# Kernel optimization log

Hardware: AMD Instinct MI355X
Metric: run time of the kernel (lower is better)

The kernel has to match this reference:

```python
import jax, jax.numpy as jnp
import numpy as np

N = 100000
E = 3200000
G = 256


def _glorot(key, shape):
    lim = float(np.sqrt(6.0 / (shape[0] + shape[1])))
    return jax.random.uniform(key, shape, jnp.float32, -lim, lim)


def setup_inputs() -> dict:
    key = jax.random.key(0)
    ks = jax.random.split(key, 16)
    x = jax.random.normal(ks[0], (N, 128), jnp.float32)
    edge_index = jax.random.randint(ks[1], (2, E), 0, N, jnp.int64)
    batch = jnp.sort(jax.random.randint(ks[2], (N,), 0, G, jnp.int64))
    inp = {
        'x': x, 'edge_index': edge_index, 'batch': batch,
        'enc_w1': _glorot(ks[3], (128, 128)), 'enc_b1': jnp.zeros((128,), jnp.float32),
        'enc_w2': _glorot(ks[4], (128, 64)),  'enc_b2': jnp.zeros((64,), jnp.float32),
        'w1': _glorot(ks[5], (64, 64)), 'b1': jnp.zeros((64,), jnp.float32),
        'w2': _glorot(ks[6], (64, 64)), 'b2': jnp.zeros((64,), jnp.float32),
        'w3': _glorot(ks[7], (64, 64)), 'b3': jnp.zeros((64,), jnp.float32),
        'sg_w': _glorot(ks[8], (64, 64)), 'sg_b': jnp.zeros((64,), jnp.float32),
        'fc1_w': _glorot(ks[9], (64, 32)), 'fc1_b': jnp.zeros((32,), jnp.float32),
        'fc2_w': _glorot(ks[10], (32, 16)), 'fc2_b': jnp.zeros((16,), jnp.float32),
        'cpd_w': _glorot(ks[11], (16, 1)), 'cpd_b': jnp.zeros((1,), jnp.float32),
        'comb_w': _glorot(ks[12], (16, 1)), 'comb_b': jnp.zeros((1,), jnp.float32),
    }
    return inp


def _gcn_edges(edge_index, n):
    # add self loops, compute symmetric normalization deg^-1/2 * deg^-1/2
    loop = jnp.arange(n, dtype=edge_index.dtype)
    src = jnp.concatenate([edge_index[0], loop])
    dst = jnp.concatenate([edge_index[1], loop])
    deg = jax.ops.segment_sum(jnp.ones_like(dst, dtype=jnp.float32), dst, num_segments=n)
    dinv = jnp.where(deg > 0, jax.lax.rsqrt(deg), 0.0)
    norm = dinv[src] * dinv[dst]  # [E+N]
    return src, dst, norm


def _propagate(h, src, dst, norm, n):
    # gather -> scale -> scatter-add (normalized neighbor aggregation)
    return jax.ops.segment_sum(h[src] * norm[:, None], dst, num_segments=n)


def _gcn_conv(h, w, b, src, dst, norm, n):
    return _propagate(h @ w, src, dst, norm, n) + b


def reference(x, edge_index, batch, enc_w1, enc_b1, enc_w2, enc_b2,
              w1, b1, w2, b2, w3, b3, sg_w, sg_b,
              fc1_w, fc1_b, fc2_w, fc2_b, cpd_w, cpd_b, comb_w, comb_b):
    n = x.shape[0]
    src, dst, norm = _gcn_edges(edge_index, n)
    # encoder
    z = jax.nn.relu(_gcn_conv(x, enc_w1, enc_b1, src, dst, norm, n))
    z = _gcn_conv(z, enc_w2, enc_b2, src, dst, norm, n)
    z = jax.nn.relu(_gcn_conv(z, w1, b1, src, dst, norm, n))
    z = jax.nn.relu(_gcn_conv(z, w2, b2, src, dst, norm, n))
    z = jax.nn.relu(_gcn_conv(z, w3, b3, src, dst, norm, n))
    for _ in range(4):
        z = _propagate(z, src, dst, norm, n)
    z = z @ sg_w + sg_b
    # global max pool over graphs
    z = jax.ops.segment_max(z, batch, num_segments=G)  # [G, 64]
    z = jax.nn.relu(z @ fc1_w + fc1_b)
    z = jax.nn.relu(z @ fc2_w + fc2_b)
    cpd_pred = z @ cpd_w + cpd_b
    comb_logits = z @ comb_w + comb_b
    return (cpd_pred, comb_logits)
```

## Files before the change

### kernel.cpp

```cpp
#include <hip/hip_runtime.h>
#include <hip/hip_fp16.h>
#include <cfloat>
#include <type_traits>

#define DEV __device__ __forceinline__

DEV unsigned enc_ord(float f) {
    unsigned u = __float_as_uint(f);
    return (u & 0x80000000u) ? ~u : (u | 0x80000000u);
}

__global__ __launch_bounds__(256) void k_bcount(const int* __restrict__ dst, int* __restrict__ bcnt, int E) {
    __shared__ int hist[256];
    int tid = threadIdx.x;
    hist[tid] = 0;
    __syncthreads();
    int base = blockIdx.x * 4096;
#pragma unroll
    for (int j = 0; j < 16; ++j) {
        int e = base + j * 256 + tid;
        if (e < E) atomicAdd(&hist[dst[e] >> 9], 1);
    }
    __syncthreads();
    if (hist[tid]) atomicAdd(&bcnt[tid], hist[tid]);
}

__global__ __launch_bounds__(256) void k_bscan(const int* __restrict__ bcnt, int* __restrict__ bbase,
                                               int* __restrict__ bcur, int* __restrict__ rowptr,
                                               int nb, int n, int E) {
    __shared__ int sh[256];
    int tid = threadIdx.x;
    int v = (tid < nb) ? bcnt[tid] : 0;
    sh[tid] = v; __syncthreads();
    for (int off = 1; off < 256; off <<= 1) {
        int x = (tid >= off) ? sh[tid - off] : 0; __syncthreads();
        sh[tid] += x; __syncthreads();
    }
    int excl = sh[tid] - v;
    if (tid < nb) { bbase[tid] = excl; bcur[tid] = excl; }
    if (tid == 0) { bbase[nb] = E; rowptr[n] = E; }
}

__global__ __launch_bounds__(256) void k_bscatter(const int* __restrict__ ei, int* __restrict__ bcur,
                                                  int2* __restrict__ pairs, int E) {
    __shared__ int hist[256];
    __shared__ int gbase[256];
    int tid = threadIdx.x;
    hist[tid] = 0;
    __syncthreads();
    int base = blockIdx.x * 4096;
    int d[16], li[16];
#pragma unroll
    for (int j = 0; j < 16; ++j) {
        int e = base + j * 256 + tid;
        if (e < E) {
            d[j] = ei[E + e];
            li[j] = atomicAdd(&hist[d[j] >> 9], 1);
        }
    }
    __syncthreads();
    if (hist[tid]) gbase[tid] = atomicAdd(&bcur[tid], hist[tid]);
    __syncthreads();
#pragma unroll
    for (int j = 0; j < 16; ++j) {
        int e = base + j * 256 + tid;
        if (e < E) {
            int b = d[j] >> 9;
            pairs[gbase[b] + li[j]] = make_int2(ei[e], d[j]);
        }
    }
}

__global__ __launch_bounds__(512) void k_bfill(const int2* __restrict__ pairs, const int* __restrict__ bbase,
                                               int* __restrict__ rowptr, float* __restrict__ dinv,
                                               int* __restrict__ colA, int n) {
    __shared__ int sdeg[512];
    __shared__ int scur[512];
    int tid = threadIdx.x;
    int b = blockIdx.x;
    int bb = bbase[b], be = bbase[b + 1];
    int nodeBase = b << 9;
    sdeg[tid] = 0;
    __syncthreads();
    for (int e = bb + tid; e < be; e += 512) {
        int2 pr = pairs[e];
        atomicAdd(&sdeg[pr.y & 511], 1);
    }
    __syncthreads();
    int v = sdeg[tid];
    __syncthreads();
    sdeg[tid] = v; __syncthreads();
    for (int off = 1; off < 512; off <<= 1) {
        int x = (tid >= off) ? sdeg[tid - off] : 0; __syncthreads();
        sdeg[tid] += x; __syncthreads();
    }
    int excl = sdeg[tid] - v;
    scur[tid] = excl;
    int node = nodeBase + tid;
    if (node < n) {
        rowptr[node] = bb + excl;
        dinv[node] = rsqrtf((float)v + 1.0f);
    }
    __syncthreads();
    for (int e = bb + tid; e < be; e += 512) {
        int2 pr = pairs[e];
        int p = atomicAdd(&scur[pr.y & 511], 1);
        colA[bb + p] = pr.x;
    }
}

template <int K, int COUT, bool SCALE, bool BIAS, typename TIN, typename TOUT>
__global__ __launch_bounds__(256) void k_mm(const TIN* __restrict__ in, const float* __restrict__ W,
                                            const float* __restrict__ bias, const float* __restrict__ dinv,
                                            TOUT* __restrict__ out, int n, int ldw, int ldo, int colOff) {
    constexpr int CG = COUT / 4;
    constexpr int SLOTS = 256 / CG;
    constexpr int TR = (K == 128) ? 32 : 64;
    constexpr int RPT = TR / SLOTS;
    constexpr int KP = K + 1;
    __shared__ __align__(16) float sW[K * COUT];
    __shared__ float sH[TR * KP];
    const int tid = threadIdx.x;
    const int rowBase = blockIdx.x * TR;

    constexpr int W4 = COUT / 4;
    for (int idx = tid; idx < K * W4; idx += 256) {
        int k = idx / W4, c4 = idx - k * W4;
        ((float4*)sW)[idx] = *(const float4*)(W + (size_t)k * ldw + colOff + c4 * 4);
    }
    if constexpr (std::is_same<TIN, float>::value) {
        const float4* inp4 = (const float4*)(in + (size_t)rowBase * K);
        for (int idx = tid; idx < TR * K / 4; idx += 256) {
            int elem = idx * 4;
            int r = elem / K, k = elem - r * K;
            float4 h = (rowBase + r < n) ? inp4[idx] : make_float4(0.f, 0.f, 0.f, 0.f);
            float* dd = &sH[r * KP + k];
            dd[0] = h.x; dd[1] = h.y; dd[2] = h.z; dd[3] = h.w;
        }
    } else {
        const uint4* inp8 = (const uint4*)(in + (size_t)rowBase * K);
        for (int idx = tid; idx < TR * K / 8; idx += 256) {
            int elem = idx * 8;
            int r = elem / K, k = elem - r * K;
            uint4 h = make_uint4(0u, 0u, 0u, 0u);
            if (rowBase + r < n) h = inp8[idx];
            const __half2* hh = (const __half2*)&h;
            float* dd = &sH[r * KP + k];
#pragma unroll
            for (int q = 0; q < 4; ++q) {
                float2 f = __half22float2(hh[q]);
                dd[2 * q] = f.x; dd[2 * q + 1] = f.y;
            }
        }
    }
    __syncthreads();

    const int cg = tid % CG;
    const int slot = tid / CG;
    float4 acc[RPT];
#pragma unroll
    for (int j = 0; j < RPT; ++j) acc[j] = make_float4(0.f, 0.f, 0.f, 0.f);
#pragma unroll 4
    for (int k = 0; k < K; ++k) {
        float4 w = *(const float4*)&sW[k * COUT + cg * 4];
#pragma unroll
        for (int j = 0; j < RPT; ++j) {
            float h = sH[(slot + j * SLOTS) * KP + k];
            acc[j].x += h * w.x; acc[j].y += h * w.y; acc[j].z += h * w.z; acc[j].w += h * w.w;
        }
    }
#pragma unroll
    for (int j = 0; j < RPT; ++j) {
        int r = rowBase + slot + j * SLOTS;
        if (r < n) {
            float4 o = acc[j];
            if (SCALE) { float di = dinv[r]; o.x *= di; o.y *= di; o.z *= di; o.w *= di; }
            if (BIAS) {
                float4 b = *(const float4*)(bias + colOff + cg * 4);
                o.x += b.x; o.y += b.y; o.z += b.z; o.w += b.w;
            }
            if constexpr (std::is_same<TOUT, float>::value) {
                *(float4*)(out + (size_t)r * ldo + colOff + cg * 4) = o;
            } else {
                __half2 p0 = __floats2half2_rn(o.x, o.y);
                __half2 p1 = __floats2half2_rn(o.z, o.w);
                uint2 st;
                st.x = *(unsigned*)&p0; st.y = *(unsigned*)&p1;
                *(uint2*)(out + (size_t)r * ldo + colOff + cg * 4) = st;
            }
        }
    }
}

template <int WIDTH, int MODE>
__global__ __launch_bounds__(256) void k_agg(const __half* __restrict__ g, const int* __restrict__ rowptr,
                                             const int* __restrict__ col, const float* __restrict__ dinv,
                                             const float* __restrict__ bias, __half* __restrict__ out, int n) {
    constexpr int LPR = WIDTH / 8;
    constexpr int RPW = 64 / LPR;
    int gw = (blockIdx.x * 256 + threadIdx.x) >> 6;
    int lane = threadIdx.x & 63;
    int seg = lane / LPR;
    int sl = lane % LPR;
    int row = gw * RPW + seg;
    if (row >= n) return;
    const uint4* g4 = (const uint4*)g + sl;
    float acc[8];
    {
        uint4 s = g4[(size_t)row * LPR];
        const __half2* h = (const __half2*)&s;
#pragma unroll
        for (int q = 0; q < 4; ++q) {
            float2 f = __half22float2(h[q]);
            acc[2 * q] = f.x; acc[2 * q + 1] = f.y;
        }
    }
    int e0 = rowptr[row], e1 = rowptr[row + 1];
    if (e0 < e1) {
        const int e1m1 = e1 - 1;
        int c[8];
#pragma unroll
        for (int j = 0; j < 8; ++j) c[j] = col[min(e0 + j, e1m1)];
        for (int eb = e0; eb < e1; eb += 8) {
            uint4 v[8];
#pragma unroll
            for (int j = 0; j < 8; ++j) v[j] = g4[(size_t)c[j] * LPR];
            int cn[8];
#pragma unroll
            for (int j = 0; j < 8; ++j) cn[j] = col[min(eb + 8 + j, e1m1)];
            int rem = e1 - eb;
#pragma unroll
            for (int j = 0; j < 8; ++j) {
                float m = (j < rem) ? 1.f : 0.f;
                const __half2* h = (const __half2*)&v[j];
#pragma unroll
                for (int q = 0; q < 4; ++q) {
                    float2 f = __half22float2(h[q]);
                    acc[2 * q]     = fmaf(m, f.x, acc[2 * q]);
                    acc[2 * q + 1] = fmaf(m, f.y, acc[2 * q + 1]);
                }
            }
#pragma unroll
            for (int j = 0; j < 8; ++j) c[j] = cn[j];
        }
    }
    float di = dinv[row];
    float r8[8];
    if (MODE == 0 || MODE == 1 || MODE == 2) {
        float4 b0 = *(const float4*)(bias + sl * 8);
        float4 b1 = *(const float4*)(bias + sl * 8 + 4);
        float bb[8] = {b0.x, b0.y, b0.z, b0.w, b1.x, b1.y, b1.z, b1.w};
#pragma unroll
        for (int t = 0; t < 8; ++t) {
            float s = di * acc[t] + bb[t];
            if (MODE == 0) r8[t] = fmaxf(s, 0.f);
            else if (MODE == 1) r8[t] = s;
            else r8[t] = di * fmaxf(s, 0.f);
        }
    } else if (MODE == 3) {
        float d2 = di * di;
#pragma unroll
        for (int t = 0; t < 8; ++t) r8[t] = acc[t] * d2;
    } else {
#pragma unroll
        for (int t = 0; t < 8; ++t) r8[t] = acc[t] * di;
    }
    uint4 o;
    __half2* oh = (__half2*)&o;
#pragma unroll
    for (int q = 0; q < 4; ++q) oh[q] = __floats2half2_rn(r8[2 * q], r8[2 * q + 1]);
    *((uint4*)out + (size_t)row * LPR + sl) = o;
}

__global__ __launch_bounds__(64) void k_pool(const float* __restrict__ z, const int* __restrict__ batch,
                                             unsigned* __restrict__ pooled, int n) {
    constexpr int ROWS = 128;
    int lane = threadIdx.x;
    int r0 = blockIdx.x * ROWS;
    if (r0 >= n) return;
    int r1 = min(r0 + ROWS, n);
    int cur = batch[r0];
    float m = -FLT_MAX;
    for (int r = r0; r < r1; ++r) {
        int b = batch[r];
        float v = z[(size_t)r * 64 + lane];
        if (b != cur) {
            atomicMax(&pooled[cur * 64 + lane], enc_ord(m));
            cur = b; m = v;
        } else {
            m = fmaxf(m, v);
        }
    }
    atomicMax(&pooled[cur * 64 + lane], enc_ord(m));
}

__global__ __launch_bounds__(256) void k_mlp(const unsigned* __restrict__ pooled,
                                             const float* __restrict__ fc1w, const float* __restrict__ fc1b,
                                             const float* __restrict__ fc2w, const float* __restrict__ fc2b,
                                             const float* __restrict__ cpdw, const float* __restrict__ cpdb,
                                             const float* __restrict__ combw, const float* __restrict__ combb,
                                             float* __restrict__ out, int G) {
    __shared__ float s1[64 * 32], s2[32 * 16], sb1[32], sb2[16], scw[16], sow[16], shead[2];
    int tid = threadIdx.x;
    for (int i = tid; i < 2048; i += 256) s1[i] = fc1w[i];
    for (int i = tid; i < 512; i += 256) s2[i] = fc2w[i];
    if (tid < 32) sb1[tid] = fc1b[tid];
    if (tid < 16) { sb2[tid] = fc2b[tid]; scw[tid] = cpdw[tid]; sow[tid] = combw[tid]; }
    if (tid == 0) { shead[0] = cpdb[0]; shead[1] = combb[0]; }
    __syncthreads();
    if (tid < G) {
        float h0[64];
#pragma unroll
        for (int k = 0; k < 64; ++k) {
            unsigned u = pooled[tid * 64 + k];
            unsigned b = (u & 0x80000000u) ? (u & 0x7fffffffu) : ~u;
            h0[k] = __uint_as_float(b);
        }
        float h1[32];
#pragma unroll
        for (int j = 0; j < 32; ++j) {
            float a = sb1[j];
#pragma unroll
            for (int k = 0; k < 64; ++k) a += h0[k] * s1[k * 32 + j];
            h1[j] = fmaxf(a, 0.f);
        }
        float h2[16];
#pragma unroll
        for (int j = 0; j < 16; ++j) {
            float a = sb2[j];
#pragma unroll
            for (int k = 0; k < 32; ++k) a += h1[k] * s2[k * 16 + j];
            h2[j] = fmaxf(a, 0.f);
        }
        float c1 = shead[0], c2 = shead[1];
#pragma unroll
        for (int k = 0; k < 16; ++k) { c1 += h2[k] * scw[k]; c2 += h2[k] * sow[k]; }
        out[tid] = c1;
        out[G + tid] = c2;
    }
}

extern "C" void kernel_launch(void* const* d_in, const int* in_sizes, int n_in,
                              void* d_out, int out_size, void* d_ws, size_t ws_size,
                              hipStream_t stream) {
    const float* x      = (const float*)d_in[0];
    const int*   ei     = (const int*)d_in[1];
    const int*   batch  = (const int*)d_in[2];
    const float* enc_w1 = (const float*)d_in[3];
    const float* enc_b1 = (const float*)d_in[4];
    const float* enc_w2 = (const float*)d_in[5];
    const float* enc_b2 = (const float*)d_in[6];
    const float* w1 = (const float*)d_in[7];   const float* b1 = (const float*)d_in[8];
    const float* w2 = (const float*)d_in[9];   const float* b2 = (const float*)d_in[10];
    const float* w3 = (const float*)d_in[11];  const float* b3 = (const float*)d_in[12];
    const float* sgw = (const float*)d_in[13]; const float* sgb = (const float*)d_in[14];
    const float* fc1w = (const float*)d_in[15]; const float* fc1b = (const float*)d_in[16];
    const float* fc2w = (const float*)d_in[17]; const float* fc2b = (const float*)d_in[18];
    const float* cpdw = (const float*)d_in[19]; const float* cpdb = (const float*)d_in[20];
    const float* combw = (const float*)d_in[21]; const float* combb = (const float*)d_in[22];

    const int n = in_sizes[0] / 128;
    const int E = in_sizes[1] / 2;
    const int G = out_size / 2;
    const int nb = (n + 511) >> 9;
    float* outp = (float*)d_out;

    char* p = (char*)d_ws;
    auto alloc = [&](size_t bytes) -> char* {
        char* r = p;
        p += (bytes + 255) & ~(size_t)255;
        return r;
    };
    int* rowptr      = (int*)alloc((size_t)(n + 1) * 4);
    float* dinv      = (float*)alloc((size_t)n * 4);
    int* bcnt        = (int*)alloc(256 * 4);
    int* bbase       = (int*)alloc(257 * 4);
    int* bcur        = (int*)alloc(256 * 4);
    int* colA        = (int*)alloc((size_t)E * 4);
    unsigned* pooled = (unsigned*)alloc((size_t)G * 64 * 4);
    __half* A        = (__half*)alloc((size_t)n * 128 * 4);
    __half* B        = (__half*)alloc((size_t)n * 128 * 2);
    float* Cf        = (float*)alloc((size_t)n * 64 * 4);
    int2* pairs      = (int2*)A;

    hipMemsetAsync(bcnt, 0, 256 * 4, stream);
    hipMemsetAsync(pooled, 0, (size_t)G * 64 * 4, stream);

    const int gE = (E + 4095) / 4096;
    k_bcount<<<gE, 256, 0, stream>>>(ei + E, bcnt, E);
    k_bscan<<<1, 256, 0, stream>>>(bcnt, bbase, bcur, rowptr, nb, n, E);
    k_bscatter<<<gE, 256, 0, stream>>>(ei, bcur, pairs, E);
    k_bfill<<<nb, 512, 0, stream>>>(pairs, bbase, rowptr, dinv, colA, n);

    const int gm128 = (n + 31) / 32;
    const int gm64  = (n + 63) / 64;
    const int ga64  = (n + 31) / 32;
    const int ga128 = (n + 15) / 16;

    k_mm<128, 64, true, false, float, __half><<<gm128, 256, 0, stream>>>(x, enc_w1, nullptr, dinv, A, n, 128, 128, 0);
    k_mm<128, 64, true, false, float, __half><<<gm128, 256, 0, stream>>>(x, enc_w1, nullptr, dinv, A, n, 128, 128, 64);
    k_agg<128, 0><<<ga128, 256, 0, stream>>>(A, rowptr, colA, dinv, enc_b1, B, n);
    k_mm<128, 64, true, false, __half, __half><<<gm128, 256, 0, stream>>>(B, enc_w2, nullptr, dinv, A, n, 64, 64, 0);
    k_agg<64, 1><<<ga64, 256, 0, stream>>>(A, rowptr, colA, dinv, enc_b2, B, n);
    k_mm<64, 64, true, false, __half, __half><<<gm64, 256, 0, stream>>>(B, w1, nullptr, dinv, A, n, 64, 64, 0);
    k_agg<64, 0><<<ga64, 256, 0, stream>>>(A, rowptr, colA, dinv, b1, B, n);
    k_mm<64, 64, true, false, __half, __half><<<gm64, 256, 0, stream>>>(B, w2, nullptr, dinv, A, n, 64, 64, 0);
    k_agg<64, 0><<<ga64, 256, 0, stream>>>(A, rowptr, colA, dinv, b2, B, n);
    k_mm<64, 64, true, false, __half, __half><<<gm64, 256, 0, stream>>>(B, w3, nullptr, dinv, A, n, 64, 64, 0);
    k_agg<64, 2><<<ga64, 256, 0, stream>>>(A, rowptr, colA, dinv, b3, B, n);
    k_agg<64, 3><<<ga64, 256, 0, stream>>>(B, rowptr, colA, dinv, b3, A, n);
    k_agg<64, 3><<<ga64, 256, 0, stream>>>(A, rowptr, colA, dinv, b3, B, n);
    k_agg<64, 3><<<ga64, 256, 0, stream>>>(B, rowptr, colA, dinv, b3, A, n);
    k_agg<64, 4><<<ga64, 256, 0, stream>>>(A, rowptr, colA, dinv, b3, B, n);
    k_mm<64, 64, false, true, __half, float><<<gm64, 256, 0, stream>>>(B, sgw, sgb, dinv, Cf, n, 64, 64, 0);
    k_pool<<<(n + 127) / 128, 64, 0, stream>>>(Cf, batch, pooled, n);
    k_mlp<<<1, 256, 0, stream>>>(pooled, fc1w, fc1b, fc2w, fc2b, cpdw, cpdb, combw, combb, outp, G);
}
```

Baseline: 1.008 ms.

## Partition CSR edges by source-node range and aggregate in cache-local phases

```diff
diff --git a/kernel.cpp b/kernel.cpp
--- a/kernel.cpp
+++ b/kernel.cpp
@@ -9,6 +9,7 @@
     unsigned u = __float_as_uint(f);
     return (u & 0x80000000u) ? ~u : (u | 0x80000000u);
 }
+
 
 __global__ __launch_bounds__(256) void k_bcount(const int* __restrict__ dst, int* __restrict__ bcnt, int E) {
     __shared__ int hist[256];
@@ -73,39 +74,46 @@
 
 __global__ __launch_bounds__(512) void k_bfill(const int2* __restrict__ pairs, const int* __restrict__ bbase,
                                                int* __restrict__ rowptr, float* __restrict__ dinv,
-                                               int* __restrict__ colA, int n) {
-    __shared__ int sdeg[512];
-    __shared__ int scur[512];
+                                               int* __restrict__ colA, int* __restrict__ pp, int n) {
+    __shared__ int sdeg2[512 * 8];
+    __shared__ int scur2[512 * 8];
+    __shared__ int ssum[512];
     int tid = threadIdx.x;
     int b = blockIdx.x;
     int bb = bbase[b], be = bbase[b + 1];
     int nodeBase = b << 9;
-    sdeg[tid] = 0;
+    for (int i = tid; i < 4096; i += 512) sdeg2[i] = 0;
     __syncthreads();
     for (int e = bb + tid; e < be; e += 512) {
         int2 pr = pairs[e];
-        atomicAdd(&sdeg[pr.y & 511], 1);
-    }
-    __syncthreads();
-    int v = sdeg[tid];
-    __syncthreads();
-    sdeg[tid] = v; __syncthreads();
+        atomicAdd(&sdeg2[(pr.y & 511) * 8 + (pr.x >> 14)], 1);
+    }
+    __syncthreads();
+    int vals[8], ex[8];
+    int tsum = 0;
+#pragma unroll
+    for (int q = 0; q < 8; ++q) { vals[q] = sdeg2[tid * 8 + q]; ex[q] = tsum; tsum += vals[q]; }
+    ssum[tid] = tsum; __syncthreads();
     for (int off = 1; off < 512; off <<= 1) {
-        int x = (tid >= off) ? sdeg[tid - off] : 0; __syncthreads();
-        sdeg[tid] += x; __syncthreads();
-    }
-    int excl = sdeg[tid] - v;
-    scur[tid] = excl;
+        int x = (tid >= off) ? ssum[tid - off] : 0; __syncthreads();
+        ssum[tid] += x; __syncthreads();
+    }
+    int excl = ssum[tid] - tsum;
+#pragma unroll
+    for (int q = 0; q < 8; ++q) scur2[tid * 8 + q] = excl + ex[q];
     int node = nodeBase + tid;
     if (node < n) {
         rowptr[node] = bb + excl;
-        dinv[node] = rsqrtf((float)v + 1.0f);
+        dinv[node] = rsqrtf((float)tsum + 1.0f);
+#pragma unroll
+        for (int q = 0; q < 8; ++q) pp[(size_t)node * 8 + q] = bb + excl + ex[q];
     }
     __syncthreads();
     for (int e = bb + tid; e < be; e += 512) {
         int2 pr = pairs[e];
-        int p = atomicAdd(&scur[pr.y & 511], 1);
-        colA[bb + p] = pr.x;
+        int idx = (pr.y & 511) * 8 + (pr.x >> 14);
+        int p2 = atomicAdd(&scur2[idx], 1);
+        colA[bb + p2] = pr.x;
     }
 }
 
@@ -192,12 +200,12 @@
     }
 }
 
-template <int WIDTH, int MODE>
-__global__ __launch_bounds__(256) void k_agg(const __half* __restrict__ g, const int* __restrict__ rowptr,
-                                             const int* __restrict__ col, const float* __restrict__ dinv,
-                                             const float* __restrict__ bias, __half* __restrict__ out, int n) {
-    constexpr int LPR = WIDTH / 8;
-    constexpr int RPW = 64 / LPR;
+template <int MODE>
+__global__ __launch_bounds__(256) void k_agg128(const __half* __restrict__ g, const int* __restrict__ rowptr,
+                                                const int* __restrict__ col, const float* __restrict__ dinv,
+                                                const float* __restrict__ bias, __half* __restrict__ out, int n) {
+    constexpr int LPR = 16;
+    constexpr int RPW = 4;
     int gw = (blockIdx.x * 256 + threadIdx.x) >> 6;
     int lane = threadIdx.x & 63;
     int seg = lane / LPR;
@@ -224,20 +232,21 @@
         for (int eb = e0; eb < e1; eb += 8) {
             uint4 v[8];
 #pragma unroll
-            for (int j = 0; j < 8; ++j) v[j] = g4[(size_t)c[j] * LPR];
+            for (int j = 0; j < 8; ++j) {
+                v[j] = make_uint4(0u, 0u, 0u, 0u);
+                if (eb + j < e1) v[j] = g4[(size_t)c[j] * LPR];
+            }
             int cn[8];
 #pragma unroll
             for (int j = 0; j < 8; ++j) cn[j] = col[min(eb + 8 + j, e1m1)];
-            int rem = e1 - eb;
 #pragma unroll
             for (int j = 0; j < 8; ++j) {
-                float m = (j < rem) ? 1.f : 0.f;
                 const __half2* h = (const __half2*)&v[j];
 #pragma unroll
                 for (int q = 0; q < 4; ++q) {
                     float2 f = __half22float2(h[q]);
-                    acc[2 * q]     = fmaf(m, f.x, acc[2 * q]);
-                    acc[2 * q + 1] = fmaf(m, f.y, acc[2 * q + 1]);
+                    acc[2 * q] += f.x;
+                    acc[2 * q + 1] += f.y;
                 }
             }
 #pragma unroll
@@ -246,30 +255,123 @@
     }
     float di = dinv[row];
     float r8[8];
-    if (MODE == 0 || MODE == 1 || MODE == 2) {
-        float4 b0 = *(const float4*)(bias + sl * 8);
-        float4 b1 = *(const float4*)(bias + sl * 8 + 4);
-        float bb[8] = {b0.x, b0.y, b0.z, b0.w, b1.x, b1.y, b1.z, b1.w};
-#pragma unroll
-        for (int t = 0; t < 8; ++t) {
-            float s = di * acc[t] + bb[t];
-            if (MODE == 0) r8[t] = fmaxf(s, 0.f);
-            else if (MODE == 1) r8[t] = s;
-            else r8[t] = di * fmaxf(s, 0.f);
-        }
-    } else if (MODE == 3) {
-        float d2 = di * di;
-#pragma unroll
-        for (int t = 0; t < 8; ++t) r8[t] = acc[t] * d2;
-    } else {
-#pragma unroll
-        for (int t = 0; t < 8; ++t) r8[t] = acc[t] * di;
+    float4 b0 = *(const float4*)(bias + sl * 8);
+    float4 b1 = *(const float4*)(bias + sl * 8 + 4);
+    float bb[8] = {b0.x, b0.y, b0.z, b0.w, b1.x, b1.y, b1.z, b1.w};
+#pragma unroll
+    for (int t = 0; t < 8; ++t) {
+        float s = di * acc[t] + bb[t];
+        r8[t] = (MODE == 0) ? fmaxf(s, 0.f) : s;
     }
     uint4 o;
     __half2* oh = (__half2*)&o;
 #pragma unroll
     for (int q = 0; q < 4; ++q) oh[q] = __floats2half2_rn(r8[2 * q], r8[2 * q + 1]);
     *((uint4*)out + (size_t)row * LPR + sl) = o;
+}
+
+template <int MODE>
+__global__ __launch_bounds__(256) void k_aggp(const __half* __restrict__ g, const int* __restrict__ pp,
+                                              const int* __restrict__ col, const float* __restrict__ dinv,
+                                              const float* __restrict__ bias, __half* __restrict__ out,
+                                              int n, int nPhases) {
+    constexpr int RPB = 224;
+    __shared__ float sacc[RPB * 64];
+    const int tid = threadIdx.x;
+    const int r0 = blockIdx.x * RPB;
+    for (int i = tid; i < RPB * 16; i += 256) {
+        int rr = i >> 4, u = i & 15;
+        int row = r0 + rr;
+        float v0 = 0.f, v1 = 0.f, v2 = 0.f, v3 = 0.f;
+        if (row < n) {
+            uint2 h = *((const uint2*)(g + (size_t)row * 64) + u);
+            __half2 a = *(__half2*)&h.x;
+            __half2 b = *(__half2*)&h.y;
+            float2 fa = __half22float2(a), fb = __half22float2(b);
+            v0 = fa.x; v1 = fa.y; v2 = fb.x; v3 = fb.y;
+        }
+        float* d = &sacc[rr * 64 + u * 4];
+        d[0] = v0; d[1] = v1; d[2] = v2; d[3] = v3;
+    }
+    __syncthreads();
+    const int segid = tid >> 3;
+    const int sl = tid & 7;
+    const uint4* g4 = (const uint4*)g + sl;
+    for (int p = 0; p < nPhases; ++p) {
+        for (int rr = segid; rr < RPB; rr += 32) {
+            int row = r0 + rr;
+            if (row >= n) break;
+            int e0 = pp[(size_t)row * 8 + p];
+            int e1 = pp[(size_t)row * 8 + p + 1];
+            if (e0 >= e1) continue;
+            const int e1m1 = e1 - 1;
+            float acc[8];
+#pragma unroll
+            for (int t = 0; t < 8; ++t) acc[t] = 0.f;
+            int c[8];
+#pragma unroll
+            for (int j = 0; j < 8; ++j) c[j] = col[min(e0 + j, e1m1)];
+            for (int eb = e0; eb < e1; eb += 8) {
+                uint4 v[8];
+#pragma unroll
+                for (int j = 0; j < 8; ++j) {
+                    v[j] = make_uint4(0u, 0u, 0u, 0u);
+                    if (eb + j < e1) v[j] = g4[(size_t)c[j] * 8];
+                }
+                int cn[8];
+#pragma unroll
+                for (int j = 0; j < 8; ++j) cn[j] = col[min(eb + 8 + j, e1m1)];
+#pragma unroll
+                for (int j = 0; j < 8; ++j) {
+                    const __half2* h = (const __half2*)&v[j];
+#pragma unroll
+                    for (int q = 0; q < 4; ++q) {
+                        float2 f = __half22float2(h[q]);
+                        acc[2 * q] += f.x;
+                        acc[2 * q + 1] += f.y;
+                    }
+                }
+#pragma unroll
+                for (int j = 0; j < 8; ++j) c[j] = cn[j];
+            }
+            float* a = &sacc[rr * 64 + sl * 8];
+#pragma unroll
+            for (int t = 0; t < 8; ++t) a[t] += acc[t];
+        }
+        __syncthreads();
+    }
+    for (int i = tid; i < RPB * 8; i += 256) {
+        int rr = i >> 3, q = i & 7;
+        int row = r0 + rr;
+        if (row >= n) break;
+        float di = dinv[row];
+        const float* a = &sacc[rr * 64 + q * 8];
+        float r8[8];
+        if (MODE <= 2) {
+            float4 b0 = *(const float4*)(bias + q * 8);
+            float4 b1 = *(const float4*)(bias + q * 8 + 4);
+            float bb[8] = {b0.x, b0.y, b0.z, b0.w, b1.x, b1.y, b1.z, b1.w};
+#pragma unroll
+            for (int t = 0; t < 8; ++t) {
+                float s = di * a[t] + bb[t];
+                if (MODE == 0) r8[t] = fmaxf(s, 0.f);
+                else if (MODE == 1) r8[t] = s;
+                else r8[t] = di * fmaxf(s, 0.f);
+            }
+        } else if (MODE == 3) {
+            float d2 = di * di;
+#pragma unroll
+            for (int t = 0; t < 8; ++t) r8[t] = a[t] * d2;
+        } else {
+#pragma unroll
+            for (int t = 0; t < 8; ++t) r8[t] = a[t] * di;
+        }
+        uint4 o;
+        __half2* oh = (__half2*)&o;
+#pragma unroll
+        for (int w = 0; w < 4; ++w) oh[w] = __floats2half2_rn(r8[2 * w], r8[2 * w + 1]);
+        *((uint4*)out + (size_t)row * 8 + q) = o;
+    }
 }
 
 __global__ __launch_bounds__(64) void k_pool(const float* __restrict__ z, const int* __restrict__ batch,
@@ -363,6 +465,7 @@
     const int E = in_sizes[1] / 2;
     const int G = out_size / 2;
     const int nb = (n + 511) >> 9;
+    const int nPhases = ((n - 1) >> 14) + 1;
     float* outp = (float*)d_out;
 
     char* p = (char*)d_ws;
@@ -377,6 +480,7 @@
     int* bbase       = (int*)alloc(257 * 4);
     int* bcur        = (int*)alloc(256 * 4);
     int* colA        = (int*)alloc((size_t)E * 4);
+    int* pp          = (int*)alloc((size_t)n * 8 * 4);
     unsigned* pooled = (unsigned*)alloc((size_t)G * 64 * 4);
     __half* A        = (__half*)alloc((size_t)n * 128 * 4);
     __half* B        = (__half*)alloc((size_t)n * 128 * 2);
@@ -390,28 +494,28 @@
     k_bcount<<<gE, 256, 0, stream>>>(ei + E, bcnt, E);
     k_bscan<<<1, 256, 0, stream>>>(bcnt, bbase, bcur, rowptr, nb, n, E);
     k_bscatter<<<gE, 256, 0, stream>>>(ei, bcur, pairs, E);
-    k_bfill<<<nb, 512, 0, stream>>>(pairs, bbase, rowptr, dinv, colA, n);
+    k_bfill<<<nb, 512, 0, stream>>>(pairs, bbase, rowptr, dinv, colA, pp, n);
 
     const int gm128 = (n + 31) / 32;
     const int gm64  = (n + 63) / 64;
-    const int ga64  = (n + 31) / 32;
     const int ga128 = (n + 15) / 16;
+    const int gp    = (n + 223) / 224;
 
     k_mm<128, 64, true, false, float, __half><<<gm128, 256, 0, stream>>>(x, enc_w1, nullptr, dinv, A, n, 128, 128, 0);
     k_mm<128, 64, true, false, float, __half><<<gm128, 256, 0, stream>>>(x, enc_w1, nullptr, dinv, A, n, 128, 128, 64);
-    k_agg<128, 0><<<ga128, 256, 0, stream>>>(A, rowptr, colA, dinv, enc_b1, B, n);
+    k_agg128<0><<<ga128, 256, 0, stream>>>(A, rowptr, colA, dinv, enc_b1, B, n);
     k_mm<128, 64, true, false, __half, __half><<<gm128, 256, 0, stream>>>(B, enc_w2, nullptr, dinv, A, n, 64, 64, 0);
-    k_agg<64, 1><<<ga64, 256, 0, stream>>>(A, rowptr, colA, dinv, enc_b2, B, n);
+    k_aggp<1><<<gp, 256, 0, stream>>>(A, pp, colA, dinv, enc_b2, B, n, nPhases);
     k_mm<64, 64, true, false, __half, __half><<<gm64, 256, 0, stream>>>(B, w1, nullptr, dinv, A, n, 64, 64, 0);
-    k_agg<64, 0><<<ga64, 256, 0, stream>>>(A, rowptr, colA, dinv, b1, B, n);
+    k_aggp<0><<<gp, 256, 0, stream>>>(A, pp, colA, dinv, b1, B, n, nPhases);
     k_mm<64, 64, true, false, __half, __half><<<gm64, 256, 0, stream>>>(B, w2, nullptr, dinv, A, n, 64, 64, 0);
-    k_agg<64, 0><<<ga64, 256, 0, stream>>>(A, rowptr, colA, dinv, b2, B, n);
+    k_aggp<0><<<gp, 256, 0, stream>>>(A, pp, colA, dinv, b2, B, n, nPhases);
     k_mm<64, 64, true, false, __half, __half><<<gm64, 256, 0, stream>>>(B, w3, nullptr, dinv, A, n, 64, 64, 0);
-    k_agg<64, 2><<<ga64, 256, 0, stream>>>(A, rowptr, colA, dinv, b3, B, n);
-    k_agg<64, 3><<<ga64, 256, 0, stream>>>(B, rowptr, colA, dinv, b3, A, n);
-    k_agg<64, 3><<<ga64, 256, 0, stream>>>(A, rowptr, colA, dinv, b3, B, n);
-    k_agg<64, 3><<<ga64, 256, 0, stream>>>(B, rowptr, colA, dinv, b3, A, n);
-    k_agg<64, 4><<<ga64, 256, 0, stream>>>(A, rowptr, colA, dinv, b3, B, n);
+    k_aggp<2><<<gp, 256, 0, stream>>>(A, pp, colA, dinv, b3, B, n, nPhases);
+    k_aggp<3><<<gp, 256, 0, stream>>>(B, pp, colA, dinv, b3, A, n, nPhases);
+    k_aggp<3><<<gp, 256, 0, stream>>>(A, pp, colA, dinv, b3, B, n, nPhases);
+    k_aggp<3><<<gp, 256, 0, stream>>>(B, pp, colA, dinv, b3, A, n, nPhases);
+    k_aggp<4><<<gp, 256, 0, stream>>>(A, pp, colA, dinv, b3, B, n, nPhases);
     k_mm<64, 64, false, true, __half, float><<<gm64, 256, 0, stream>>>(B, sgw, sgb, dinv, Cf, n, 64, 64, 0);
     k_pool<<<(n + 127) / 128, 64, 0, stream>>>(Cf, batch, pooled, n);
     k_mlp<<<1, 256, 0, stream>>>(pooled, fc1w, fc1b, fc2w, fc2b, cpdw, cpdb, combw, combb, outp, G);
```

Result: slower. 1.576 ms (+56.3%).

## Partition CSR edges by source window and process them in phases for gather locality

Applied to the files above, without the earlier changes.

```diff
diff --git a/kernel.cpp b/kernel.cpp
--- a/kernel.cpp
+++ b/kernel.cpp
@@ -10,6 +10,7 @@
     return (u & 0x80000000u) ? ~u : (u | 0x80000000u);
 }
 
+
 __global__ __launch_bounds__(256) void k_bcount(const int* __restrict__ dst, int* __restrict__ bcnt, int E) {
     __shared__ int hist[256];
     int tid = threadIdx.x;
@@ -26,8 +27,7 @@
 }
 
 __global__ __launch_bounds__(256) void k_bscan(const int* __restrict__ bcnt, int* __restrict__ bbase,
-                                               int* __restrict__ bcur, int* __restrict__ rowptr,
-                                               int nb, int n, int E) {
+                                               int* __restrict__ bcur, int nb, int E) {
     __shared__ int sh[256];
     int tid = threadIdx.x;
     int v = (tid < nb) ? bcnt[tid] : 0;
@@ -38,7 +38,7 @@
     }
     int excl = sh[tid] - v;
     if (tid < nb) { bbase[tid] = excl; bcur[tid] = excl; }
-    if (tid == 0) { bbase[nb] = E; rowptr[n] = E; }
+    if (tid == 0) bbase[nb] = E;
 }
 
 __global__ __launch_bounds__(256) void k_bscatter(const int* __restrict__ ei, int* __restrict__ bcur,
@@ -72,40 +72,48 @@
 }
 
 __global__ __launch_bounds__(512) void k_bfill(const int2* __restrict__ pairs, const int* __restrict__ bbase,
-                                               int* __restrict__ rowptr, float* __restrict__ dinv,
-                                               int* __restrict__ colA, int n) {
-    __shared__ int sdeg[512];
-    __shared__ int scur[512];
+                                               float* __restrict__ dinv, int* __restrict__ colA,
+                                               int* __restrict__ pp, int n, int nw) {
+    __shared__ int sdeg2[512 * 16];
+    __shared__ int ssum[512];
     int tid = threadIdx.x;
     int b = blockIdx.x;
     int bb = bbase[b], be = bbase[b + 1];
     int nodeBase = b << 9;
-    sdeg[tid] = 0;
+    for (int i = tid; i < 512 * 16; i += 512) sdeg2[i] = 0;
     __syncthreads();
     for (int e = bb + tid; e < be; e += 512) {
         int2 pr = pairs[e];
-        atomicAdd(&sdeg[pr.y & 511], 1);
-    }
-    __syncthreads();
-    int v = sdeg[tid];
-    __syncthreads();
-    sdeg[tid] = v; __syncthreads();
+        atomicAdd(&sdeg2[(pr.y & 511) * 16 + (pr.x >> 13)], 1);
+    }
+    __syncthreads();
+    int vals[16], ex[16];
+    int tsum = 0;
+#pragma unroll
+    for (int q = 0; q < 16; ++q) {
+        vals[q] = (q < nw) ? sdeg2[tid * 16 + q] : 0;
+        ex[q] = tsum; tsum += vals[q];
+    }
+    ssum[tid] = tsum; __syncthreads();
     for (int off = 1; off < 512; off <<= 1) {
-        int x = (tid >= off) ? sdeg[tid - off] : 0; __syncthreads();
-        sdeg[tid] += x; __syncthreads();
-    }
-    int excl = sdeg[tid] - v;
-    scur[tid] = excl;
+        int x = (tid >= off) ? ssum[tid - off] : 0; __syncthreads();
+        ssum[tid] += x; __syncthreads();
+    }
+    int excl = ssum[tid] - tsum;
+#pragma unroll
+    for (int q = 0; q < 16; ++q) if (q < nw) sdeg2[tid * 16 + q] = excl + ex[q];
     int node = nodeBase + tid;
     if (node < n) {
-        rowptr[node] = bb + excl;
-        dinv[node] = rsqrtf((float)v + 1.0f);
+        dinv[node] = rsqrtf((float)tsum + 1.0f);
+        for (int q = 0; q < nw; ++q) pp[node * 16 + q] = bb + excl + ex[q];
+        pp[node * 16 + nw] = bb + excl + tsum;
     }
     __syncthreads();
     for (int e = bb + tid; e < be; e += 512) {
         int2 pr = pairs[e];
-        int p = atomicAdd(&scur[pr.y & 511], 1);
-        colA[bb + p] = pr.x;
+        int idx = (pr.y & 511) * 16 + (pr.x >> 13);
+        int p2 = atomicAdd(&sdeg2[idx], 1);
+        colA[bb + p2] = pr.x;
     }
 }
 
@@ -193,83 +201,103 @@
 }
 
 template <int WIDTH, int MODE>
-__global__ __launch_bounds__(256) void k_agg(const __half* __restrict__ g, const int* __restrict__ rowptr,
-                                             const int* __restrict__ col, const float* __restrict__ dinv,
-                                             const float* __restrict__ bias, __half* __restrict__ out, int n) {
+__global__ __launch_bounds__(256) void k_aggp(const __half* __restrict__ g, const int* __restrict__ pp,
+                                              const int* __restrict__ col, const float* __restrict__ dinv,
+                                              const float* __restrict__ bias, __half* __restrict__ out,
+                                              int n, int nw) {
     constexpr int LPR = WIDTH / 8;
-    constexpr int RPW = 64 / LPR;
-    int gw = (blockIdx.x * 256 + threadIdx.x) >> 6;
-    int lane = threadIdx.x & 63;
-    int seg = lane / LPR;
-    int sl = lane % LPR;
-    int row = gw * RPW + seg;
-    if (row >= n) return;
+    constexpr int SPW = 64 / LPR;
+    constexpr int RPW = SPW * 4;
+    constexpr int MERGE = (WIDTH == 64) ? 2 : 1;
+    const int tid = threadIdx.x;
+    const int wave = tid >> 6, lane = tid & 63;
+    const int seg = lane / LPR, sl = lane % LPR;
+    const int rowBase = blockIdx.x * (RPW * 4) + wave * RPW + seg * 4;
     const uint4* g4 = (const uint4*)g + sl;
-    float acc[8];
-    {
-        uint4 s = g4[(size_t)row * LPR];
+
+    float acc[4][8];
+#pragma unroll
+    for (int j = 0; j < 4; ++j) {
+        int row = rowBase + j;
+        uint4 s = make_uint4(0u, 0u, 0u, 0u);
+        if (row < n) s = g4[(size_t)row * LPR];
         const __half2* h = (const __half2*)&s;
 #pragma unroll
         for (int q = 0; q < 4; ++q) {
             float2 f = __half22float2(h[q]);
-            acc[2 * q] = f.x; acc[2 * q + 1] = f.y;
-        }
-    }
-    int e0 = rowptr[row], e1 = rowptr[row + 1];
-    if (e0 < e1) {
-        const int e1m1 = e1 - 1;
-        int c[8];
-#pragma unroll
-        for (int j = 0; j < 8; ++j) c[j] = col[min(e0 + j, e1m1)];
-        for (int eb = e0; eb < e1; eb += 8) {
-            uint4 v[8];
-#pragma unroll
-            for (int j = 0; j < 8; ++j) v[j] = g4[(size_t)c[j] * LPR];
-            int cn[8];
-#pragma unroll
-            for (int j = 0; j < 8; ++j) cn[j] = col[min(eb + 8 + j, e1m1)];
-            int rem = e1 - eb;
-#pragma unroll
-            for (int j = 0; j < 8; ++j) {
-                float m = (j < rem) ? 1.f : 0.f;
-                const __half2* h = (const __half2*)&v[j];
-#pragma unroll
-                for (int q = 0; q < 4; ++q) {
-                    float2 f = __half22float2(h[q]);
-                    acc[2 * q]     = fmaf(m, f.x, acc[2 * q]);
-                    acc[2 * q + 1] = fmaf(m, f.y, acc[2 * q + 1]);
+            acc[j][2 * q] = f.x; acc[j][2 * q + 1] = f.y;
+        }
+    }
+
+    const int nPh = (nw + MERGE - 1) / MERGE;
+    for (int p = 0; p < nPh; ++p) {
+        const int lo = p * MERGE;
+        const int hi = min(lo + MERGE, nw);
+#pragma unroll
+        for (int j = 0; j < 4; ++j) {
+            int row = rowBase + j;
+            if (row < n) {
+                int e0 = pp[row * 16 + lo];
+                int e1 = pp[row * 16 + hi];
+                if (e0 < e1) {
+                    const int e1m1 = e1 - 1;
+                    for (int eb = e0; eb < e1; eb += 8) {
+                        int cc[8];
+#pragma unroll
+                        for (int t = 0; t < 8; ++t) cc[t] = col[min(eb + t, e1m1)];
+                        uint4 v[8];
+#pragma unroll
+                        for (int t = 0; t < 8; ++t) {
+                            v[t] = make_uint4(0u, 0u, 0u, 0u);
+                            if (eb + t < e1) v[t] = g4[(size_t)cc[t] * LPR];
+                        }
+#pragma unroll
+                        for (int t = 0; t < 8; ++t) {
+                            const __half2* h = (const __half2*)&v[t];
+#pragma unroll
+                            for (int q = 0; q < 4; ++q) {
+                                float2 f = __half22float2(h[q]);
+                                acc[j][2 * q] += f.x;
+                                acc[j][2 * q + 1] += f.y;
+                            }
+                        }
+                    }
                 }
             }
-#pragma unroll
-            for (int j = 0; j < 8; ++j) c[j] = cn[j];
-        }
-    }
-    float di = dinv[row];
-    float r8[8];
-    if (MODE == 0 || MODE == 1 || MODE == 2) {
-        float4 b0 = *(const float4*)(bias + sl * 8);
-        float4 b1 = *(const float4*)(bias + sl * 8 + 4);
-        float bb[8] = {b0.x, b0.y, b0.z, b0.w, b1.x, b1.y, b1.z, b1.w};
-#pragma unroll
-        for (int t = 0; t < 8; ++t) {
-            float s = di * acc[t] + bb[t];
-            if (MODE == 0) r8[t] = fmaxf(s, 0.f);
-            else if (MODE == 1) r8[t] = s;
-            else r8[t] = di * fmaxf(s, 0.f);
-        }
-    } else if (MODE == 3) {
-        float d2 = di * di;
-#pragma unroll
-        for (int t = 0; t < 8; ++t) r8[t] = acc[t] * d2;
-    } else {
-#pragma unroll
-        for (int t = 0; t < 8; ++t) r8[t] = acc[t] * di;
-    }
-    uint4 o;
-    __half2* oh = (__half2*)&o;
-#pragma unroll
-    for (int q = 0; q < 4; ++q) oh[q] = __floats2half2_rn(r8[2 * q], r8[2 * q + 1]);
-    *((uint4*)out + (size_t)row * LPR + sl) = o;
+        }
+    }
+
+#pragma unroll
+    for (int j = 0; j < 4; ++j) {
+        int row = rowBase + j;
+        if (row >= n) continue;
+        float di = dinv[row];
+        float r8[8];
+        if (MODE <= 2) {
+            float4 b0 = *(const float4*)(bias + sl * 8);
+            float4 b1 = *(const float4*)(bias + sl * 8 + 4);
+            float bb[8] = {b0.x, b0.y, b0.z, b0.w, b1.x, b1.y, b1.z, b1.w};
+#pragma unroll
+            for (int t = 0; t < 8; ++t) {
+                float s = di * acc[j][t] + bb[t];
+                if (MODE == 0) r8[t] = fmaxf(s, 0.f);
+                else if (MODE == 1) r8[t] = s;
+                else r8[t] = di * fmaxf(s, 0.f);
+            }
+        } else if (MODE == 3) {
+            float d2 = di * di;
+#pragma unroll
+            for (int t = 0; t < 8; ++t) r8[t] = acc[j][t] * d2;
+        } else {
+#pragma unroll
+            for (int t = 0; t < 8; ++t) r8[t] = acc[j][t] * di;
+        }
+        uint4 o;
+        __half2* oh = (__half2*)&o;
+#pragma unroll
+        for (int q = 0; q < 4; ++q) oh[q] = __floats2half2_rn(r8[2 * q], r8[2 * q + 1]);
+        *((uint4*)out + (size_t)row * LPR + sl) = o;
+    }
 }
 
 __global__ __launch_bounds__(64) void k_pool(const float* __restrict__ z, const int* __restrict__ batch,
@@ -363,6 +391,7 @@
     const int E = in_sizes[1] / 2;
     const int G = out_size / 2;
     const int nb = (n + 511) >> 9;
+    const int nw = ((n - 1) >> 13) + 1;
     float* outp = (float*)d_out;
 
     char* p = (char*)d_ws;
@@ -371,12 +400,12 @@
         p += (bytes + 255) & ~(size_t)255;
         return r;
     };
-    int* rowptr      = (int*)alloc((size_t)(n + 1) * 4);
     float* dinv      = (float*)alloc((size_t)n * 4);
     int* bcnt        = (int*)alloc(256 * 4);
     int* bbase       = (int*)alloc(257 * 4);
     int* bcur        = (int*)alloc(256 * 4);
     int* colA        = (int*)alloc((size_t)E * 4);
+    int* pp          = (int*)alloc((size_t)n * 16 * 4);
     unsigned* pooled = (unsigned*)alloc((size_t)G * 64 * 4);
     __half* A        = (__half*)alloc((size_t)n * 128 * 4);
     __half* B        = (__half*)alloc((size_t)n * 128 * 2);
@@ -388,30 +417,30 @@
 
     const int gE = (E + 4095) / 4096;
     k_bcount<<<gE, 256, 0, stream>>>(ei + E, bcnt, E);
-    k_bscan<<<1, 256, 0, stream>>>(bcnt, bbase, bcur, rowptr, nb, n, E);
+    k_bscan<<<1, 256, 0, stream>>>(bcnt, bbase, bcur, nb, E);
     k_bscatter<<<gE, 256, 0, stream>>>(ei, bcur, pairs, E);
-    k_bfill<<<nb, 512, 0, stream>>>(pairs, bbase, rowptr, dinv, colA, n);
+    k_bfill<<<nb, 512, 0, stream>>>(pairs, bbase, dinv, colA, pp, n, nw);
 
     const int gm128 = (n + 31) / 32;
     const int gm64  = (n + 63) / 64;
-    const int ga64  = (n + 31) / 32;
-    const int ga128 = (n + 15) / 16;
+    const int ga64  = (n + 127) / 128;
+    const int ga128 = (n + 63) / 64;
 
     k_mm<128, 64, true, false, float, __half><<<gm128, 256, 0, stream>>>(x, enc_w1, nullptr, dinv, A, n, 128, 128, 0);
     k_mm<128, 64, true, false, float, __half><<<gm128, 256, 0, stream>>>(x, enc_w1, nullptr, dinv, A, n, 128, 128, 64);
-    k_agg<128, 0><<<ga128, 256, 0, stream>>>(A, rowptr, colA, dinv, enc_b1, B, n);
+    k_aggp<128, 0><<<ga128, 256, 0, stream>>>(A, pp, colA, dinv, enc_b1, B, n, nw);
     k_mm<128, 64, true, false, __half, __half><<<gm128, 256, 0, stream>>>(B, enc_w2, nullptr, dinv, A, n, 64, 64, 0);
-    k_agg<64, 1><<<ga64, 256, 0, stream>>>(A, rowptr, colA, dinv, enc_b2, B, n);
+    k_aggp<64, 1><<<ga64, 256, 0, stream>>>(A, pp, colA, dinv, enc_b2, B, n, nw);
     k_mm<64, 64, true, false, __half, __half><<<gm64, 256, 0, stream>>>(B, w1, nullptr, dinv, A, n, 64, 64, 0);
-    k_agg<64, 0><<<ga64, 256, 0, stream>>>(A, rowptr, colA, dinv, b1, B, n);
+    k_aggp<64, 0><<<ga64, 256, 0, stream>>>(A, pp, colA, dinv, b1, B, n, nw);
     k_mm<64, 64, true, false, __half, __half><<<gm64, 256, 0, stream>>>(B, w2, nullptr, dinv, A, n, 64, 64, 0);
-    k_agg<64, 0><<<ga64, 256, 0, stream>>>(A, rowptr, colA, dinv, b2, B, n);
+    k_aggp<64, 0><<<ga64, 256, 0, stream>>>(A, pp, colA, dinv, b2, B, n, nw);
     k_mm<64, 64, true, false, __half, __half><<<gm64, 256, 0, stream>>>(B, w3, nullptr, dinv, A, n, 64, 64, 0);
-    k_agg<64, 2><<<ga64, 256, 0, stream>>>(A, rowptr, colA, dinv, b3, B, n);
-    k_agg<64, 3><<<ga64, 256, 0, stream>>>(B, rowptr, colA, dinv, b3, A, n);
-    k_agg<64, 3><<<ga64, 256, 0, stream>>>(A, rowptr, colA, dinv, b3, B, n);
-    k_agg<64, 3><<<ga64, 256, 0, stream>>>(B, rowptr, colA, dinv, b3, A, n);
-    k_agg<64, 4><<<ga64, 256, 0, stream>>>(A, rowptr, colA, dinv, b3, B, n);
+    k_aggp<64, 2><<<ga64, 256, 0, stream>>>(A, pp, colA, dinv, b3, B, n, nw);
+    k_aggp<64, 3><<<ga64, 256, 0, stream>>>(B, pp, colA, dinv, b3, A, n, nw);
+    k_aggp<64, 3><<<ga64, 256, 0, stream>>>(A, pp, colA, dinv, b3, B, n, nw);
+    k_aggp<64, 3><<<ga64, 256, 0, stream>>>(B, pp, colA, dinv, b3, A, n, nw);
+    k_aggp<64, 4><<<ga64, 256, 0, stream>>>(A, pp, colA, dinv, b3, B, n, nw);
     k_mm<64, 64, false, true, __half, float><<<gm64, 256, 0, stream>>>(B, sgw, sgb, dinv, Cf, n, 64, 64, 0);
     k_pool<<<(n + 127) / 128, 64, 0, stream>>>(Cf, batch, pooled, n);
     k_mlp<<<1, 256, 0, stream>>>(pooled, fc1w, fc1b, fc2w, fc2b, cpdw, cpdb, combw, combb, outp, G);
```

Measured after the change: 1.384 ms. 37.2% more time.
